# Performance work log

Measured on AMD Instinct MI355X. Metric: run time of the kernel, lower is better.

## Reference

```python
import jax, jax.numpy as jnp
import numpy as np

BLOCK_SIZE = 32
# E2M1 (FP4) representable magnitudes and rounding midpoints
FP4_GRID = jnp.array([0.0, 0.5, 1.0, 1.5, 2.0, 3.0, 4.0, 6.0], dtype=jnp.float32)
FP4_MIDS = jnp.array([0.25, 0.75, 1.25, 1.75, 2.5, 3.5, 5.0], dtype=jnp.float32)


def quantize_to_mxfp4(w, block_size=BLOCK_SIZE):
    """Quantize (K, N) weight to MXFP4: per-block-of-32 (along K) power-of-2 scale
    + E2M1 codes. Returns dequantized-code tensor q (K//bs, bs, N) and scales
    (K//bs, 1, N) so that dequant = q * scales."""
    K, N = w.shape
    wb = w.reshape(K // block_size, block_size, N)
    amax = jnp.max(jnp.abs(wb), axis=1, keepdims=True)          # (K//bs, 1, N)
    # E8M0 scale: 2^(floor(log2(amax)) - 2) so amax/scale falls in [4, 8) -> clipped to 6
    exp = jnp.floor(jnp.log2(jnp.maximum(amax, 1e-30))) - 2.0
    scales = jnp.exp2(exp)
    x = wb / scales
    idx = jnp.digitize(jnp.abs(x), FP4_MIDS)                    # round-to-nearest FP4 magnitude
    q = jnp.sign(x) * FP4_GRID[idx]
    return q, scales


def mxfp4_matmul(inputs, q, scales, block_size=BLOCK_SIZE):
    """inputs: (..., K); q: (K//bs, bs, N); scales: (K//bs, 1, N)."""
    K = inputs.shape[-1]
    N = q.shape[-1]
    w = (q * scales).reshape(K, N)   # fused dequant (reference form)
    return inputs @ w


def setup_inputs() -> dict:
    key = jax.random.key(0)
    ks = jax.random.split(key, 3)
    B, S, D, F = 4, 2048, 2048, 8192
    inputs = jax.random.normal(ks[0], (B, S, D), dtype=jnp.float32)
    up_kernel = jax.random.normal(ks[1], (D, F), dtype=jnp.float32) * (1.0 / np.sqrt(D))
    down_kernel = jax.random.normal(ks[2], (F, D), dtype=jnp.float32) * (1.0 / np.sqrt(F))
    up_bias = jnp.zeros((F,), dtype=jnp.float32)
    down_bias = jnp.zeros((D,), dtype=jnp.float32)
    return {"inputs": inputs, "up_kernel": up_kernel, "up_bias": up_bias,
            "down_kernel": down_kernel, "down_bias": down_bias}


def reference(inputs, up_kernel, up_bias, down_kernel, down_bias):
    q_up, s_up = quantize_to_mxfp4(up_kernel, BLOCK_SIZE)
    x = mxfp4_matmul(inputs, q_up, s_up, BLOCK_SIZE) + up_bias
    x = jax.nn.gelu(x)
    q_dn, s_dn = quantize_to_mxfp4(down_kernel, BLOCK_SIZE)
    x = mxfp4_matmul(x, q_dn, s_dn, BLOCK_SIZE) + down_bias
    return x
```

## Files before the change

kernel.cpp:

```cpp
#include <hip/hip_runtime.h>
#include <hip/hip_bf16.h>

typedef __bf16 bf16_t;
typedef __attribute__((ext_vector_type(8))) __bf16 bf16x8;
typedef __attribute__((ext_vector_type(4))) float f32x4;
typedef __attribute__((ext_vector_type(4))) unsigned int u32x4;

__device__ __forceinline__ void gload_lds16(const bf16_t* g, bf16_t* l) {
    __builtin_amdgcn_global_load_lds(
        (const __attribute__((address_space(1))) void*)g,
        (__attribute__((address_space(3))) void*)l,
        16, 0, 0);
}

__device__ __forceinline__ float gelu_f(float v) {
    float u = 0.7978845608028654f * (v + 0.044715f * v * v * v);
    float e = __expf(-2.f * u);
    float t = __fdividef(1.f - e, 1.f + e);
    return 0.5f * v * (1.f + t);
}

__global__ void cvt_kernel(const float* __restrict__ in, bf16_t* __restrict__ out, int n) {
    int i = (blockIdx.x * blockDim.x + threadIdx.x) << 3;
    if (i >= n) return;
    const f32x4* p = (const f32x4*)(in + i);
    f32x4 a = __builtin_nontemporal_load(p);
    f32x4 b = __builtin_nontemporal_load(p + 1);
    bf16x8 o;
    o[0] = (bf16_t)a[0]; o[1] = (bf16_t)a[1]; o[2] = (bf16_t)a[2]; o[3] = (bf16_t)a[3];
    o[4] = (bf16_t)b[0]; o[5] = (bf16_t)b[1]; o[6] = (bf16_t)b[2]; o[7] = (bf16_t)b[3];
    *(bf16x8*)(out + i) = o;
}

__global__ void quantize_kernel(const float* __restrict__ w, bf16_t* __restrict__ wt,
                                int K, int N) {
    int tid = blockIdx.x * blockDim.x + threadIdx.x;
    int total = (K >> 5) * N;
    if (tid >= total) return;
    int n = tid % N;
    int b = tid / N;
    const float* src = w + (size_t)b * 32 * N + n;
    float v[32];
    float amax = 0.f;
#pragma unroll
    for (int i = 0; i < 32; ++i) {
        v[i] = __builtin_nontemporal_load(src + (size_t)i * N);
        amax = fmaxf(amax, fabsf(v[i]));
    }
    unsigned eb = (__float_as_uint(amax) >> 23) & 0xFF;
    float scale = __uint_as_float((eb - 2u) << 23);
    float inv   = __uint_as_float((256u - eb) << 23);
    if (amax == 0.f) { scale = 0.f; inv = 0.f; }
    bf16_t dq[32];
#pragma unroll
    for (int i = 0; i < 32; ++i) {
        float x  = v[i] * inv;
        float ax = fabsf(x);
        float q = ax < 0.25f ? 0.0f : ax < 0.75f ? 0.5f : ax < 1.25f ? 1.0f :
                  ax < 1.75f ? 1.5f : ax < 2.5f  ? 2.0f : ax < 3.5f  ? 3.0f :
                  ax < 5.0f  ? 4.0f : 6.0f;
        float d = copysignf(q * scale, x);
        dq[i] = (bf16_t)d;
    }
    bf16_t* dst = wt + (size_t)n * K + b * 32;
#pragma unroll
    for (int j = 0; j < 4; ++j) {
        bf16x8 p;
#pragma unroll
        for (int t = 0; t < 8; ++t) p[t] = dq[j * 8 + t];
        *(bf16x8*)(dst + j * 8) = p;
    }
}

#define VMW4  asm volatile("s_waitcnt vmcnt(4)" ::: "memory")
#define VMW0  asm volatile("s_waitcnt vmcnt(0)" ::: "memory")
#define BARR  asm volatile("s_barrier" ::: "memory")
#define LGKM0 asm volatile("s_waitcnt lgkmcnt(0)" ::: "memory")

#define MFMA_ROW(MI, A0, A1)                                                          \
    acc[MI][0] = __builtin_amdgcn_mfma_f32_16x16x32_bf16(A0, bf00, acc[MI][0],0,0,0); \
    acc[MI][0] = __builtin_amdgcn_mfma_f32_16x16x32_bf16(A1, bf01, acc[MI][0],0,0,0); \
    acc[MI][1] = __builtin_amdgcn_mfma_f32_16x16x32_bf16(A0, bf10, acc[MI][1],0,0,0); \
    acc[MI][1] = __builtin_amdgcn_mfma_f32_16x16x32_bf16(A1, bf11, acc[MI][1],0,0,0); \
    acc[MI][2] = __builtin_amdgcn_mfma_f32_16x16x32_bf16(A0, bf20, acc[MI][2],0,0,0); \
    acc[MI][2] = __builtin_amdgcn_mfma_f32_16x16x32_bf16(A1, bf21, acc[MI][2],0,0,0); \
    acc[MI][3] = __builtin_amdgcn_mfma_f32_16x16x32_bf16(A0, bf30, acc[MI][3],0,0,0); \
    acc[MI][3] = __builtin_amdgcn_mfma_f32_16x16x32_bf16(A1, bf31, acc[MI][3],0,0,0);

#define PHASE(BUF, P, STAGE_STMT, TAIL_STMT)                                          \
  {                                                                                   \
    af00 = lda(BUF, 2*(P),   0); af01 = lda(BUF, 2*(P),   1);                         \
    af10 = lda(BUF, 2*(P)+1, 0); af11 = lda(BUF, 2*(P)+1, 1);                         \
    if ((P) == 0) {                                                                   \
      bf00 = ldb(BUF,0,0); bf01 = ldb(BUF,0,1);                                       \
      bf10 = ldb(BUF,1,0); bf11 = ldb(BUF,1,1);                                       \
      bf20 = ldb(BUF,2,0); bf21 = ldb(BUF,2,1);                                       \
      bf30 = ldb(BUF,3,0); bf31 = ldb(BUF,3,1);                                       \
    }                                                                                 \
    STAGE_STMT;                                                                       \
    BARR;                                                                             \
    LGKM0;                                                                            \
    __builtin_amdgcn_s_setprio(1);                                                    \
    MFMA_ROW(2*(P),   af00, af01);                                                    \
    MFMA_ROW(2*(P)+1, af10, af11);                                                    \
    __builtin_amdgcn_s_setprio(0);                                                    \
    TAIL_STMT;                                                                        \
    BARR;                                                                             \
  }

template <int EPI, int MAP>
__global__ __launch_bounds__(512, 2)
void gemm_kernel(const bf16_t* __restrict__ A, const bf16_t* __restrict__ Bt,
                 const float* __restrict__ bias, void* __restrict__ Cout,
                 int M, int N, int K) {
    __shared__ __align__(16) char smem[131072];
    bf16_t* sAp = (bf16_t*)smem;
    bf16_t* sBp = (bf16_t*)(smem + 65536);
    const int tid     = threadIdx.x;
    const int lane    = tid & 63;
    const int wv      = tid >> 6;
    const int wr      = wv >> 2;
    const int wc      = wv & 3;
    const int laneLow = lane & 15;
    const int laneHi  = lane >> 4;

    int bm, bn;
    const int bid = blockIdx.x;
    if (MAP == 1) {
        const int xcd = bid & 7;
        const int l   = bid >> 3;
        const int r   = l >> 5;
        const int u   = l & 31;
        bm = r * 8 + ((xcd >> 2) << 2) + (u >> 3);
        bn = ((xcd & 3) << 3) + (u & 7);
    } else {
        const int ntn = N >> 8;
        const int nwg = gridDim.x;
        int wg  = (bid & 7) * (nwg >> 3) + (bid >> 3);
        bm = wg / ntn; bn = wg % ntn;
    }

    const int sr8 = lane >> 3;
    const int swz = (((lane & 7) ^ sr8) << 3);
    const bf16_t* aSrc = A  + (size_t)(bm * 256 + wv * 8 + sr8) * K + swz;
    const bf16_t* bSrc = Bt + (size_t)(bn * 256 + wv * 8 + sr8) * K + swz;

    auto stageA = [&](int b, int kt, int h) {
        const bf16_t* s = aSrc + (size_t)(h * 128) * K + kt * 64;
        gload_lds16(s,                &sAp[b * 16384 + (h * 128 + wv * 8) * 64]);
        gload_lds16(s + (size_t)64*K, &sAp[b * 16384 + (h * 128 + 64 + wv * 8) * 64]);
    };
    auto stageB = [&](int b, int kt, int h) {
        const bf16_t* s = bSrc + (size_t)(h * 128) * K + kt * 64;
        gload_lds16(s,                &sBp[b * 16384 + (h * 128 + wv * 8) * 64]);
        gload_lds16(s + (size_t)64*K, &sBp[b * 16384 + (h * 128 + 64 + wv * 8) * 64]);
    };

    const int s7  = laneLow & 7;
    const int xk0 = ((laneHi) ^ s7) << 3;
    const int xk1 = ((4 + laneHi) ^ s7) << 3;
    const int aOffBase = (wr * 128 + laneLow) * 64;
    const int bOffBase = (wc * 64 + laneLow) * 64;
    auto lda = [&](int b, int m, int ks) -> bf16x8 {
        return *(const bf16x8*)(&sAp[b * 16384 + aOffBase + m * 1024 + (ks ? xk1 : xk0)]);
    };
    auto ldb = [&](int b, int n2, int ks) -> bf16x8 {
        return *(const bf16x8*)(&sBp[b * 16384 + bOffBase + n2 * 1024 + (ks ? xk1 : xk0)]);
    };

    f32x4 acc[8][4];
#pragma unroll
    for (int i = 0; i < 8; ++i)
#pragma unroll
        for (int j = 0; j < 4; ++j) acc[i][j] = (f32x4){0.f, 0.f, 0.f, 0.f};

    bf16x8 af00, af01, af10, af11;
    bf16x8 bf00, bf01, bf10, bf11, bf20, bf21, bf30, bf31;

    stageA(0, 0, 0); stageA(0, 0, 1);
    stageB(0, 0, 0); stageB(0, 0, 1);
    stageB(1, 1, 0); stageB(1, 1, 1);
    VMW4;
    BARR;

    const int niter = K >> 7;
    for (int i = 0; i < niter; ++i) {
        const bool nlast = (i + 1 < niter);
        const int kO  = 2 * i + 1;
        const int kN  = 2 * i + 2;
        const int kN1 = 2 * i + 3;
        PHASE(0, 0, stageA(1, kO, 0), ((void)0));
        PHASE(0, 1, stageA(1, kO, 1), ((void)0));
        PHASE(0, 2, if (nlast) stageB(0, kN, 0), ((void)0));
        PHASE(0, 3, if (nlast) stageB(0, kN, 1),
              if (nlast) { VMW4; } else { VMW0; });
        PHASE(1, 0, if (nlast) stageA(0, kN, 0), ((void)0));
        PHASE(1, 1, if (nlast) stageA(0, kN, 1), ((void)0));
        PHASE(1, 2, if (nlast) stageB(1, kN1, 0), ((void)0));
        PHASE(1, 3, if (nlast) stageB(1, kN1, 1),
              if (nlast) { VMW4; });
    }

    if (EPI == 0) {
        bf16_t* sC = (bf16_t*)smem;
#pragma unroll
        for (int n = 0; n < 4; ++n) {
            const int colL = wc * 64 + n * 16 + laneLow;
            const float bv = bias[bn * 256 + colL];
#pragma unroll
            for (int m = 0; m < 8; ++m) {
#pragma unroll
                for (int j = 0; j < 4; ++j) {
                    const int rowL = wr * 128 + m * 16 + (laneHi << 2) + j;
                    float v = acc[m][n][j] + bv;
                    int byte = (rowL << 9) + (colL << 1);
                    byte ^= ((rowL >> 2) & 3) << 5;
                    *(bf16_t*)((char*)sC + byte) = (bf16_t)gelu_f(v);
                }
            }
        }
        LGKM0;
        BARR;
        bf16_t* Cb = (bf16_t*)Cout;
        const size_t rb = (size_t)bm * 256, cb = (size_t)bn * 256;
#pragma unroll
        for (int s = 0; s < 16; ++s) {
            const int row = s * 16 + (tid >> 5);
            int byte = (row << 9) + ((tid & 31) << 4);
            byte ^= ((row >> 2) & 3) << 5;
            u32x4 v = *(const u32x4*)((char*)sC + byte);
            __builtin_nontemporal_store(
                v, (u32x4*)(&Cb[(rb + row) * N + cb + ((tid & 31) << 3)]));
        }
    } else {
        const int r0 = bm * 256 + wr * 128 + (laneHi << 2);
        const int c0 = bn * 256 + wc * 64 + laneLow;
        float* Cf = (float*)Cout;
#pragma unroll
        for (int n = 0; n < 4; ++n) {
            const int col = c0 + n * 16;
            const float bv = bias[col];
#pragma unroll
            for (int m = 0; m < 8; ++m) {
#pragma unroll
                for (int j = 0; j < 4; ++j) {
                    const int row = r0 + m * 16 + j;
                    __builtin_nontemporal_store(acc[m][n][j] + bv,
                                                &Cf[(size_t)row * N + col]);
                }
            }
        }
    }
}

extern "C" void kernel_launch(void* const* d_in, const int* in_sizes, int n_in,
                              void* d_out, int out_size, void* d_ws, size_t ws_size,
                              hipStream_t stream) {
    const float* inputs = (const float*)d_in[0];
    const float* up_w   = (const float*)d_in[1];
    const float* up_b   = (const float*)d_in[2];
    const float* dn_w   = (const float*)d_in[3];
    const float* dn_b   = (const float*)d_in[4];
    float* out = (float*)d_out;

    const int D = in_sizes[4];
    const int F = in_sizes[2];
    const int M = in_sizes[0] / D;

    size_t r0_bytes = (size_t)(M > F ? M : F) * D * 2;
    char* ws = (char*)d_ws;
    bf16_t* in_bf = (bf16_t*)ws;
    bf16_t* wdn_t = (bf16_t*)ws;
    bf16_t* wup_t = (bf16_t*)(ws + r0_bytes);
    bf16_t* mid   = (bf16_t*)(ws + r0_bytes + (size_t)F * D * 2);

    int ncvt = M * D;
    cvt_kernel<<<(ncvt / 8 + 255) / 256, 256, 0, stream>>>(inputs, in_bf, ncvt);
    int qup = (D / 32) * F;
    quantize_kernel<<<(qup + 255) / 256, 256, 0, stream>>>(up_w, wup_t, D, F);
    gemm_kernel<0, 1><<<(M / 256) * (F / 256), 512, 0, stream>>>(
        in_bf, wup_t, up_b, (void*)mid, M, F, D);
    int qdn = (F / 32) * D;
    quantize_kernel<<<(qdn + 255) / 256, 256, 0, stream>>>(dn_w, wdn_t, F, D);
    gemm_kernel<1, 0><<<(M / 256) * (D / 256), 512, 0, stream>>>(
        mid, wdn_t, dn_b, (void*)out, M, D, F);
}
```

Measured before the change: 548.1 us.

## Fuse prep kernels and overlap down-weight quantization with up GEMM

Merges the input bf16 conversion and up-weight quantization into one launch. The down-weight quantization now runs as 512 extra workgroups appended to the up-projection GEMM grid, writing to a separate workspace region so it can overlap with the GEMM instead of running as its own serial kernel. This removes two launches and the idle gap between them. In exchange, the extra blocks compete with the GEMM for CUs, use a lot of workspace, and could delay GEMM tail blocks or change their scheduling order.

After: 555.6 us. No clear change (+1.4%).

```diff
diff --git a/kernel.cpp b/kernel.cpp
--- a/kernel.cpp
+++ b/kernel.cpp
@@ -20,25 +20,11 @@
     return 0.5f * v * (1.f + t);
 }
 
-__global__ void cvt_kernel(const float* __restrict__ in, bf16_t* __restrict__ out, int n) {
-    int i = (blockIdx.x * blockDim.x + threadIdx.x) << 3;
-    if (i >= n) return;
-    const f32x4* p = (const f32x4*)(in + i);
-    f32x4 a = __builtin_nontemporal_load(p);
-    f32x4 b = __builtin_nontemporal_load(p + 1);
-    bf16x8 o;
-    o[0] = (bf16_t)a[0]; o[1] = (bf16_t)a[1]; o[2] = (bf16_t)a[2]; o[3] = (bf16_t)a[3];
-    o[4] = (bf16_t)b[0]; o[5] = (bf16_t)b[1]; o[6] = (bf16_t)b[2]; o[7] = (bf16_t)b[3];
-    *(bf16x8*)(out + i) = o;
-}
-
-__global__ void quantize_kernel(const float* __restrict__ w, bf16_t* __restrict__ wt,
-                                int K, int N) {
-    int tid = blockIdx.x * blockDim.x + threadIdx.x;
-    int total = (K >> 5) * N;
-    if (tid >= total) return;
-    int n = tid % N;
-    int b = tid / N;
+__device__ __forceinline__ void quant_one(const float* __restrict__ w,
+                                          bf16_t* __restrict__ wt,
+                                          int K, int N, int tix) {
+    int n = tix % N;
+    int b = tix / N;
     const float* src = w + (size_t)b * 32 * N + n;
     float v[32];
     float amax = 0.f;
@@ -69,6 +55,28 @@
 #pragma unroll
         for (int t = 0; t < 8; ++t) p[t] = dq[j * 8 + t];
         *(bf16x8*)(dst + j * 8) = p;
+    }
+}
+
+__global__ void prep_kernel(const float* __restrict__ in, bf16_t* __restrict__ out,
+                            int ncvt, int cvtBlocks,
+                            const float* __restrict__ upw, bf16_t* __restrict__ upwt,
+                            int K, int N) {
+    int bid = blockIdx.x;
+    if (bid < cvtBlocks) {
+        int i = (bid * blockDim.x + threadIdx.x) << 3;
+        if (i >= ncvt) return;
+        const f32x4* p = (const f32x4*)(in + i);
+        f32x4 a = __builtin_nontemporal_load(p);
+        f32x4 b = __builtin_nontemporal_load(p + 1);
+        bf16x8 o;
+        o[0] = (bf16_t)a[0]; o[1] = (bf16_t)a[1]; o[2] = (bf16_t)a[2]; o[3] = (bf16_t)a[3];
+        o[4] = (bf16_t)b[0]; o[5] = (bf16_t)b[1]; o[6] = (bf16_t)b[2]; o[7] = (bf16_t)b[3];
+        *(bf16x8*)(out + i) = o;
+    } else {
+        int tix = (bid - cvtBlocks) * blockDim.x + threadIdx.x;
+        if (tix >= (K >> 5) * N) return;
+        quant_one(upw, upwt, K, N, tix);
     }
 }
 
@@ -108,15 +116,26 @@
     BARR;                                                                             \
   }
 
-template <int EPI, int MAP>
+template <int EPI, int MAP, int XQ>
 __global__ __launch_bounds__(512, 2)
 void gemm_kernel(const bf16_t* __restrict__ A, const bf16_t* __restrict__ Bt,
                  const float* __restrict__ bias, void* __restrict__ Cout,
-                 int M, int N, int K) {
+                 int M, int N, int K,
+                 const float* __restrict__ qw, bf16_t* __restrict__ qwt,
+                 int qK, int qN, int gemmBlocks) {
     __shared__ __align__(16) char smem[131072];
+    const int tid = threadIdx.x;
+
+    if (XQ && (int)blockIdx.x >= gemmBlocks) {
+        const int total  = (qK >> 5) * qN;
+        const int stride = (gridDim.x - gemmBlocks) * 512;
+        for (int tix = (blockIdx.x - gemmBlocks) * 512 + tid; tix < total; tix += stride)
+            quant_one(qw, qwt, qK, qN, tix);
+        return;
+    }
+
     bf16_t* sAp = (bf16_t*)smem;
     bf16_t* sBp = (bf16_t*)(smem + 65536);
-    const int tid     = threadIdx.x;
     const int lane    = tid & 63;
     const int wv      = tid >> 6;
     const int wr      = wv >> 2;
@@ -135,7 +154,7 @@
         bn = ((xcd & 3) << 3) + (u & 7);
     } else {
         const int ntn = N >> 8;
-        const int nwg = gridDim.x;
+        const int nwg = gemmBlocks;
         int wg  = (bid & 7) * (nwg >> 3) + (bid >> 3);
         bm = wg / ntn; bn = wg % ntn;
     }
@@ -275,13 +294,19 @@
     bf16_t* mid   = (bf16_t*)(ws + r0_bytes + (size_t)F * D * 2);
 
     int ncvt = M * D;
-    cvt_kernel<<<(ncvt / 8 + 255) / 256, 256, 0, stream>>>(inputs, in_bf, ncvt);
-    int qup = (D / 32) * F;
-    quantize_kernel<<<(qup + 255) / 256, 256, 0, stream>>>(up_w, wup_t, D, F);
-    gemm_kernel<0, 1><<<(M / 256) * (F / 256), 512, 0, stream>>>(
-        in_bf, wup_t, up_b, (void*)mid, M, F, D);
-    int qdn = (F / 32) * D;
-    quantize_kernel<<<(qdn + 255) / 256, 256, 0, stream>>>(dn_w, wdn_t, F, D);
-    gemm_kernel<1, 0><<<(M / 256) * (D / 256), 512, 0, stream>>>(
-        mid, wdn_t, dn_b, (void*)out, M, D, F);
-}
+    int cvtBlocks = ncvt / (8 * 256);
+    int qupBlocks = ((D / 32) * F + 255) / 256;
+    prep_kernel<<<cvtBlocks + qupBlocks, 256, 0, stream>>>(
+        inputs, in_bf, ncvt, cvtBlocks, up_w, wup_t, D, F);
+
+    int gemmBlocks = (M / 256) * (F / 256);
+    bf16_t* wdn_t2 = (bf16_t*)(ws + r0_bytes + (size_t)F * D * 2 + (size_t)M * F * 2);
+    gemm_kernel<0, 1, 1><<<gemmBlocks + 512, 512, 0, stream>>>(
+        in_bf, wup_t, up_b, (void*)mid, M, F, D,
+        dn_w, wdn_t2, F, D, gemmBlocks);
+
+    gemm_kernel<1, 0, 0><<<(M / 256) * (D / 256), 512, 0, stream>>>(
+        mid, wdn_t2, dn_b, (void*)out, M, D, F,
+        nullptr, nullptr, 0, 0, 256);
+    (void)wdn_t; (void)ws_size; (void)n_in; (void)out_size;
+}
```

## Merge prep kernels and make up-projection GEMM persistent over M segments

Applied to the files above, without the earlier changes.

The cast and both weight quantizations are merged into one prep launch, with the down weights moved to their own workspace region so they no longer alias the input buffer. The first GEMM becomes a persistent kernel of 256 blocks. Each block keeps a fixed N column tile and its B stream across four M tiles, with an XCD-aware mapping, and writes GELU output after every 16 K-iterations. The aim is fewer launches and better B reuse in L2. In exchange, the epilogue now does direct scattered 2-byte nontemporal stores instead of the LDS-staged 16-byte stores, which risks poorer write coalescing. The persistent kernel also hardcodes the loop counts and grid size to the test shapes.

Measured after the change: 556.4 us. About the same (+1.5%).

```diff
diff --git a/kernel.cpp b/kernel.cpp
--- a/kernel.cpp
+++ b/kernel.cpp
@@ -20,25 +20,11 @@
     return 0.5f * v * (1.f + t);
 }
 
-__global__ void cvt_kernel(const float* __restrict__ in, bf16_t* __restrict__ out, int n) {
-    int i = (blockIdx.x * blockDim.x + threadIdx.x) << 3;
-    if (i >= n) return;
-    const f32x4* p = (const f32x4*)(in + i);
-    f32x4 a = __builtin_nontemporal_load(p);
-    f32x4 b = __builtin_nontemporal_load(p + 1);
-    bf16x8 o;
-    o[0] = (bf16_t)a[0]; o[1] = (bf16_t)a[1]; o[2] = (bf16_t)a[2]; o[3] = (bf16_t)a[3];
-    o[4] = (bf16_t)b[0]; o[5] = (bf16_t)b[1]; o[6] = (bf16_t)b[2]; o[7] = (bf16_t)b[3];
-    *(bf16x8*)(out + i) = o;
-}
-
-__global__ void quantize_kernel(const float* __restrict__ w, bf16_t* __restrict__ wt,
-                                int K, int N) {
-    int tid = blockIdx.x * blockDim.x + threadIdx.x;
-    int total = (K >> 5) * N;
-    if (tid >= total) return;
-    int n = tid % N;
-    int b = tid / N;
+__device__ __forceinline__ void quant_one(const float* __restrict__ w,
+                                          bf16_t* __restrict__ wt,
+                                          int K, int N, int tix) {
+    int n = tix % N;
+    int b = tix / N;
     const float* src = w + (size_t)b * 32 * N + n;
     float v[32];
     float amax = 0.f;
@@ -69,6 +55,34 @@
 #pragma unroll
         for (int t = 0; t < 8; ++t) p[t] = dq[j * 8 + t];
         *(bf16x8*)(dst + j * 8) = p;
+    }
+}
+
+__global__ void prep_kernel(const float* __restrict__ in, bf16_t* __restrict__ out,
+                            int ncvt, int cvtB,
+                            const float* __restrict__ upw, bf16_t* __restrict__ upwt,
+                            int upK, int upN, int qupB,
+                            const float* __restrict__ dnw, bf16_t* __restrict__ dnwt,
+                            int dnK, int dnN) {
+    int bid = blockIdx.x;
+    if (bid < cvtB) {
+        int i = (bid * blockDim.x + threadIdx.x) << 3;
+        if (i >= ncvt) return;
+        const f32x4* p = (const f32x4*)(in + i);
+        f32x4 a = __builtin_nontemporal_load(p);
+        f32x4 b = __builtin_nontemporal_load(p + 1);
+        bf16x8 o;
+        o[0] = (bf16_t)a[0]; o[1] = (bf16_t)a[1]; o[2] = (bf16_t)a[2]; o[3] = (bf16_t)a[3];
+        o[4] = (bf16_t)b[0]; o[5] = (bf16_t)b[1]; o[6] = (bf16_t)b[2]; o[7] = (bf16_t)b[3];
+        *(bf16x8*)(out + i) = o;
+    } else if (bid < cvtB + qupB) {
+        int tix = (bid - cvtB) * blockDim.x + threadIdx.x;
+        if (tix >= (upK >> 5) * upN) return;
+        quant_one(upw, upwt, upK, upN, tix);
+    } else {
+        int tix = (bid - cvtB - qupB) * blockDim.x + threadIdx.x;
+        if (tix >= (dnK >> 5) * dnN) return;
+        quant_one(dnw, dnwt, dnK, dnN, tix);
     }
 }
 
@@ -108,6 +122,110 @@
     BARR;                                                                             \
   }
 
+__global__ __launch_bounds__(512, 2)
+void gemm1_persistent(const bf16_t* __restrict__ A, const bf16_t* __restrict__ Bt,
+                      const float* __restrict__ bias, bf16_t* __restrict__ C,
+                      int M, int N, int K) {
+    __shared__ __align__(16) char smem[131072];
+    bf16_t* sAp = (bf16_t*)smem;
+    bf16_t* sBp = (bf16_t*)(smem + 65536);
+    const int tid     = threadIdx.x;
+    const int lane    = tid & 63;
+    const int wv      = tid >> 6;
+    const int wr      = wv >> 2;
+    const int wc      = wv & 3;
+    const int laneLow = lane & 15;
+    const int laneHi  = lane >> 4;
+
+    const int bid = blockIdx.x;
+    const int xcd = bid & 7, q = bid >> 3;
+    const int bn  = ((xcd & 3) << 3) + (q & 7);
+    const int bm0 = ((xcd >> 2) << 2) + (q >> 3);
+
+    const int sr8 = lane >> 3;
+    const int swz = (((lane & 7) ^ sr8) << 3);
+    const size_t aTh = (size_t)(wv * 8 + sr8) * K + swz;
+    const bf16_t* bSrc = Bt + (size_t)(bn * 256 + wv * 8 + sr8) * K + swz;
+
+    auto stageA = [&](int b, int t, int h) {
+        const bf16_t* s = A + (size_t)(bm0 + ((t >> 5) << 3)) * (size_t)(256 * K)
+                            + aTh + (size_t)(h * 128) * K + (t & 31) * 64;
+        gload_lds16(s,                &sAp[b * 16384 + (h * 128 + wv * 8) * 64]);
+        gload_lds16(s + (size_t)64*K, &sAp[b * 16384 + (h * 128 + 64 + wv * 8) * 64]);
+    };
+    auto stageB = [&](int b, int t, int h) {
+        const bf16_t* s = bSrc + (size_t)(h * 128) * K + (t & 31) * 64;
+        gload_lds16(s,                &sBp[b * 16384 + (h * 128 + wv * 8) * 64]);
+        gload_lds16(s + (size_t)64*K, &sBp[b * 16384 + (h * 128 + 64 + wv * 8) * 64]);
+    };
+
+    const int s7  = laneLow & 7;
+    const int xk0 = ((laneHi) ^ s7) << 3;
+    const int xk1 = ((4 + laneHi) ^ s7) << 3;
+    const int aOffBase = (wr * 128 + laneLow) * 64;
+    const int bOffBase = (wc * 64 + laneLow) * 64;
+    auto lda = [&](int b, int m, int ks) -> bf16x8 {
+        return *(const bf16x8*)(&sAp[b * 16384 + aOffBase + m * 1024 + (ks ? xk1 : xk0)]);
+    };
+    auto ldb = [&](int b, int n2, int ks) -> bf16x8 {
+        return *(const bf16x8*)(&sBp[b * 16384 + bOffBase + n2 * 1024 + (ks ? xk1 : xk0)]);
+    };
+
+    f32x4 acc[8][4];
+#pragma unroll
+    for (int i = 0; i < 8; ++i)
+#pragma unroll
+        for (int j = 0; j < 4; ++j) acc[i][j] = (f32x4){0.f, 0.f, 0.f, 0.f};
+
+    bf16x8 af00, af01, af10, af11;
+    bf16x8 bf00, bf01, bf10, bf11, bf20, bf21, bf30, bf31;
+
+    stageA(0, 0, 0); stageA(0, 0, 1);
+    stageB(0, 0, 0); stageB(0, 0, 1);
+    stageB(1, 1, 0); stageB(1, 1, 1);
+    VMW4;
+    BARR;
+
+    const int c0 = bn * 256 + wc * 64 + laneLow;
+#pragma unroll 1
+    for (int g = 0; g < 64; ++g) {
+        const bool nl = (g < 63);
+        const int tA1 = 2 * g + 1, tN = 2 * g + 2, tN1 = 2 * g + 3;
+        PHASE(0, 0, stageA(1, tA1, 0), ((void)0));
+        PHASE(0, 1, stageA(1, tA1, 1), ((void)0));
+        PHASE(0, 2, if (nl) stageB(0, tN, 0), ((void)0));
+        PHASE(0, 3, if (nl) stageB(0, tN, 1),
+              if (nl) { VMW4; } else { VMW0; });
+        PHASE(1, 0, if (nl) stageA(0, tN, 0), ((void)0));
+        PHASE(1, 1, if (nl) stageA(0, tN, 1), ((void)0));
+        PHASE(1, 2, if (nl) stageB(1, tN1, 0), ((void)0));
+        PHASE(1, 3, if (nl) stageB(1, tN1, 1),
+              if (nl) { VMW4; });
+
+        if ((g & 15) == 15) {
+            const int seg = g >> 4;
+            const int r0 = (bm0 + (seg << 3)) * 256 + wr * 128 + (laneHi << 2);
+#pragma unroll
+            for (int n = 0; n < 4; ++n) {
+                const int col = c0 + n * 16;
+                const float bv = bias[col];
+#pragma unroll
+                for (int m = 0; m < 8; ++m) {
+#pragma unroll
+                    for (int j = 0; j < 4; ++j) {
+                        const int row = r0 + m * 16 + j;
+                        bf16_t h = (bf16_t)gelu_f(acc[m][n][j] + bv);
+                        __builtin_nontemporal_store(
+                            __builtin_bit_cast(short, h),
+                            (short*)&C[(size_t)row * N + col]);
+                    }
+                    acc[m][n] = (f32x4){0.f, 0.f, 0.f, 0.f};
+                }
+            }
+        }
+    }
+}
+
 template <int EPI, int MAP>
 __global__ __launch_bounds__(512, 2)
 void gemm_kernel(const bf16_t* __restrict__ A, const bf16_t* __restrict__ Bt,
@@ -201,38 +319,7 @@
               if (nlast) { VMW4; });
     }
 
-    if (EPI == 0) {
-        bf16_t* sC = (bf16_t*)smem;
-#pragma unroll
-        for (int n = 0; n < 4; ++n) {
-            const int colL = wc * 64 + n * 16 + laneLow;
-            const float bv = bias[bn * 256 + colL];
-#pragma unroll
-            for (int m = 0; m < 8; ++m) {
-#pragma unroll
-                for (int j = 0; j < 4; ++j) {
-                    const int rowL = wr * 128 + m * 16 + (laneHi << 2) + j;
-                    float v = acc[m][n][j] + bv;
-                    int byte = (rowL << 9) + (colL << 1);
-                    byte ^= ((rowL >> 2) & 3) << 5;
-                    *(bf16_t*)((char*)sC + byte) = (bf16_t)gelu_f(v);
-                }
-            }
-        }
-        LGKM0;
-        BARR;
-        bf16_t* Cb = (bf16_t*)Cout;
-        const size_t rb = (size_t)bm * 256, cb = (size_t)bn * 256;
-#pragma unroll
-        for (int s = 0; s < 16; ++s) {
-            const int row = s * 16 + (tid >> 5);
-            int byte = (row << 9) + ((tid & 31) << 4);
-            byte ^= ((row >> 2) & 3) << 5;
-            u32x4 v = *(const u32x4*)((char*)sC + byte);
-            __builtin_nontemporal_store(
-                v, (u32x4*)(&Cb[(rb + row) * N + cb + ((tid & 31) << 3)]));
-        }
-    } else {
+    {
         const int r0 = bm * 256 + wr * 128 + (laneHi << 2);
         const int c0 = bn * 256 + wc * 64 + laneLow;
         float* Cf = (float*)Cout;
@@ -270,18 +357,23 @@
     size_t r0_bytes = (size_t)(M > F ? M : F) * D * 2;
     char* ws = (char*)d_ws;
     bf16_t* in_bf = (bf16_t*)ws;
-    bf16_t* wdn_t = (bf16_t*)ws;
     bf16_t* wup_t = (bf16_t*)(ws + r0_bytes);
     bf16_t* mid   = (bf16_t*)(ws + r0_bytes + (size_t)F * D * 2);
+    bf16_t* wdn_t = (bf16_t*)(ws + r0_bytes + (size_t)F * D * 2 + (size_t)M * F * 2);
 
     int ncvt = M * D;
-    cvt_kernel<<<(ncvt / 8 + 255) / 256, 256, 0, stream>>>(inputs, in_bf, ncvt);
-    int qup = (D / 32) * F;
-    quantize_kernel<<<(qup + 255) / 256, 256, 0, stream>>>(up_w, wup_t, D, F);
-    gemm_kernel<0, 1><<<(M / 256) * (F / 256), 512, 0, stream>>>(
-        in_bf, wup_t, up_b, (void*)mid, M, F, D);
-    int qdn = (F / 32) * D;
-    quantize_kernel<<<(qdn + 255) / 256, 256, 0, stream>>>(dn_w, wdn_t, F, D);
+    int cvtB = ncvt / (8 * 256);
+    int qupB = ((D / 32) * F + 255) / 256;
+    int qdnB = ((F / 32) * D + 255) / 256;
+    prep_kernel<<<cvtB + qupB + qdnB, 256, 0, stream>>>(
+        inputs, in_bf, ncvt, cvtB,
+        up_w, wup_t, D, F, qupB,
+        dn_w, wdn_t, F, D);
+
+    gemm1_persistent<<<256, 512, 0, stream>>>(
+        in_bf, wup_t, up_b, mid, M, F, D);
+
     gemm_kernel<1, 0><<<(M / 256) * (D / 256), 512, 0, stream>>>(
         mid, wdn_t, dn_b, (void*)out, M, D, F);
-}
+    (void)ws_size; (void)n_in; (void)out_size;
+}
```

## Switch GEMM to 32x32x16 MFMA tiles and merge prep kernels into one launch

Applied to the files above, without the earlier changes.

The GEMM inner loop moves from 16x16x32 bf16 MFMAs to 32x32x16 MFMAs. Each wave's 128x64 tile is now 4x2 blocks of 32x32, which cuts LDS fragment reads per MFMA FLOP and changes the LDS read addressing and the epilogue row mapping. The input cast and both weight quantizations now run in a single prep kernel, saving launches and letting the down-weight quantize overlap the other prep work. The cost is a separate workspace region for the down weights, plus a risk of LDS bank conflicts under the new swizzle use.

Measured after the change: 589.6 us. 7.6% more time.

```diff
diff --git a/kernel.cpp b/kernel.cpp
--- a/kernel.cpp
+++ b/kernel.cpp
@@ -4,6 +4,7 @@
 typedef __bf16 bf16_t;
 typedef __attribute__((ext_vector_type(8))) __bf16 bf16x8;
 typedef __attribute__((ext_vector_type(4))) float f32x4;
+typedef __attribute__((ext_vector_type(16))) float f32x16;
 typedef __attribute__((ext_vector_type(4))) unsigned int u32x4;
 
 __device__ __forceinline__ void gload_lds16(const bf16_t* g, bf16_t* l) {
@@ -20,25 +21,11 @@
     return 0.5f * v * (1.f + t);
 }
 
-__global__ void cvt_kernel(const float* __restrict__ in, bf16_t* __restrict__ out, int n) {
-    int i = (blockIdx.x * blockDim.x + threadIdx.x) << 3;
-    if (i >= n) return;
-    const f32x4* p = (const f32x4*)(in + i);
-    f32x4 a = __builtin_nontemporal_load(p);
-    f32x4 b = __builtin_nontemporal_load(p + 1);
-    bf16x8 o;
-    o[0] = (bf16_t)a[0]; o[1] = (bf16_t)a[1]; o[2] = (bf16_t)a[2]; o[3] = (bf16_t)a[3];
-    o[4] = (bf16_t)b[0]; o[5] = (bf16_t)b[1]; o[6] = (bf16_t)b[2]; o[7] = (bf16_t)b[3];
-    *(bf16x8*)(out + i) = o;
-}
-
-__global__ void quantize_kernel(const float* __restrict__ w, bf16_t* __restrict__ wt,
-                                int K, int N) {
-    int tid = blockIdx.x * blockDim.x + threadIdx.x;
-    int total = (K >> 5) * N;
-    if (tid >= total) return;
-    int n = tid % N;
-    int b = tid / N;
+__device__ __forceinline__ void quant_one(const float* __restrict__ w,
+                                          bf16_t* __restrict__ wt,
+                                          int K, int N, int tix) {
+    int n = tix % N;
+    int b = tix / N;
     const float* src = w + (size_t)b * 32 * N + n;
     float v[32];
     float amax = 0.f;
@@ -72,37 +59,61 @@
     }
 }
 
+__global__ void prep_kernel(const float* __restrict__ in, bf16_t* __restrict__ out,
+                            int ncvt, int cvtB,
+                            const float* __restrict__ upw, bf16_t* __restrict__ upwt,
+                            int upK, int upN, int qupB,
+                            const float* __restrict__ dnw, bf16_t* __restrict__ dnwt,
+                            int dnK, int dnN) {
+    int bid = blockIdx.x;
+    if (bid < cvtB) {
+        int i = (bid * blockDim.x + threadIdx.x) << 3;
+        if (i >= ncvt) return;
+        const f32x4* p = (const f32x4*)(in + i);
+        f32x4 a = __builtin_nontemporal_load(p);
+        f32x4 b = __builtin_nontemporal_load(p + 1);
+        bf16x8 o;
+        o[0] = (bf16_t)a[0]; o[1] = (bf16_t)a[1]; o[2] = (bf16_t)a[2]; o[3] = (bf16_t)a[3];
+        o[4] = (bf16_t)b[0]; o[5] = (bf16_t)b[1]; o[6] = (bf16_t)b[2]; o[7] = (bf16_t)b[3];
+        *(bf16x8*)(out + i) = o;
+    } else if (bid < cvtB + qupB) {
+        int tix = (bid - cvtB) * blockDim.x + threadIdx.x;
+        if (tix >= (upK >> 5) * upN) return;
+        quant_one(upw, upwt, upK, upN, tix);
+    } else {
+        int tix = (bid - cvtB - qupB) * blockDim.x + threadIdx.x;
+        if (tix >= (dnK >> 5) * dnN) return;
+        quant_one(dnw, dnwt, dnK, dnN, tix);
+    }
+}
+
 #define VMW4  asm volatile("s_waitcnt vmcnt(4)" ::: "memory")
 #define VMW0  asm volatile("s_waitcnt vmcnt(0)" ::: "memory")
 #define BARR  asm volatile("s_barrier" ::: "memory")
 #define LGKM0 asm volatile("s_waitcnt lgkmcnt(0)" ::: "memory")
 
-#define MFMA_ROW(MI, A0, A1)                                                          \
-    acc[MI][0] = __builtin_amdgcn_mfma_f32_16x16x32_bf16(A0, bf00, acc[MI][0],0,0,0); \
-    acc[MI][0] = __builtin_amdgcn_mfma_f32_16x16x32_bf16(A1, bf01, acc[MI][0],0,0,0); \
-    acc[MI][1] = __builtin_amdgcn_mfma_f32_16x16x32_bf16(A0, bf10, acc[MI][1],0,0,0); \
-    acc[MI][1] = __builtin_amdgcn_mfma_f32_16x16x32_bf16(A1, bf11, acc[MI][1],0,0,0); \
-    acc[MI][2] = __builtin_amdgcn_mfma_f32_16x16x32_bf16(A0, bf20, acc[MI][2],0,0,0); \
-    acc[MI][2] = __builtin_amdgcn_mfma_f32_16x16x32_bf16(A1, bf21, acc[MI][2],0,0,0); \
-    acc[MI][3] = __builtin_amdgcn_mfma_f32_16x16x32_bf16(A0, bf30, acc[MI][3],0,0,0); \
-    acc[MI][3] = __builtin_amdgcn_mfma_f32_16x16x32_bf16(A1, bf31, acc[MI][3],0,0,0);
+#define MFMA32(A, B, C) __builtin_amdgcn_mfma_f32_32x32x16_bf16(A, B, C, 0, 0, 0)
 
 #define PHASE(BUF, P, STAGE_STMT, TAIL_STMT)                                          \
   {                                                                                   \
-    af00 = lda(BUF, 2*(P),   0); af01 = lda(BUF, 2*(P),   1);                         \
-    af10 = lda(BUF, 2*(P)+1, 0); af11 = lda(BUF, 2*(P)+1, 1);                         \
+    af0 = lda(BUF, P, 0); af1 = lda(BUF, P, 1);                                       \
+    af2 = lda(BUF, P, 2); af3 = lda(BUF, P, 3);                                       \
     if ((P) == 0) {                                                                   \
-      bf00 = ldb(BUF,0,0); bf01 = ldb(BUF,0,1);                                       \
-      bf10 = ldb(BUF,1,0); bf11 = ldb(BUF,1,1);                                       \
-      bf20 = ldb(BUF,2,0); bf21 = ldb(BUF,2,1);                                       \
-      bf30 = ldb(BUF,3,0); bf31 = ldb(BUF,3,1);                                       \
+      bf00 = ldb(BUF,0,0); bf01 = ldb(BUF,0,1); bf02 = ldb(BUF,0,2); bf03 = ldb(BUF,0,3); \
+      bf10 = ldb(BUF,1,0); bf11 = ldb(BUF,1,1); bf12 = ldb(BUF,1,2); bf13 = ldb(BUF,1,3); \
     }                                                                                 \
     STAGE_STMT;                                                                       \
     BARR;                                                                             \
     LGKM0;                                                                            \
     __builtin_amdgcn_s_setprio(1);                                                    \
-    MFMA_ROW(2*(P),   af00, af01);                                                    \
-    MFMA_ROW(2*(P)+1, af10, af11);                                                    \
+    acc[P][0] = MFMA32(af0, bf00, acc[P][0]);                                         \
+    acc[P][1] = MFMA32(af0, bf10, acc[P][1]);                                         \
+    acc[P][0] = MFMA32(af1, bf01, acc[P][0]);                                         \
+    acc[P][1] = MFMA32(af1, bf11, acc[P][1]);                                         \
+    acc[P][0] = MFMA32(af2, bf02, acc[P][0]);                                         \
+    acc[P][1] = MFMA32(af2, bf12, acc[P][1]);                                         \
+    acc[P][0] = MFMA32(af3, bf03, acc[P][0]);                                         \
+    acc[P][1] = MFMA32(af3, bf13, acc[P][1]);                                         \
     __builtin_amdgcn_s_setprio(0);                                                    \
     TAIL_STMT;                                                                        \
     BARR;                                                                             \
@@ -116,13 +127,13 @@
     __shared__ __align__(16) char smem[131072];
     bf16_t* sAp = (bf16_t*)smem;
     bf16_t* sBp = (bf16_t*)(smem + 65536);
-    const int tid     = threadIdx.x;
-    const int lane    = tid & 63;
-    const int wv      = tid >> 6;
-    const int wr      = wv >> 2;
-    const int wc      = wv & 3;
-    const int laneLow = lane & 15;
-    const int laneHi  = lane >> 4;
+    const int tid    = threadIdx.x;
+    const int lane   = tid & 63;
+    const int wv     = tid >> 6;
+    const int wr     = wv >> 2;
+    const int wc     = wv & 3;
+    const int lane31 = lane & 31;
+    const int laneHi2 = lane >> 5;
 
     int bm, bn;
     const int bid = blockIdx.x;
@@ -156,26 +167,28 @@
         gload_lds16(s + (size_t)64*K, &sBp[b * 16384 + (h * 128 + 64 + wv * 8) * 64]);
     };
 
-    const int s7  = laneLow & 7;
-    const int xk0 = ((laneHi) ^ s7) << 3;
-    const int xk1 = ((4 + laneHi) ^ s7) << 3;
-    const int aOffBase = (wr * 128 + laneLow) * 64;
-    const int bOffBase = (wc * 64 + laneLow) * 64;
-    auto lda = [&](int b, int m, int ks) -> bf16x8 {
-        return *(const bf16x8*)(&sAp[b * 16384 + aOffBase + m * 1024 + (ks ? xk1 : xk0)]);
+    const int s7 = lane31 & 7;
+    auto lda = [&](int b, int mt, int k) -> bf16x8 {
+        const int row = wr * 128 + mt * 32 + lane31;
+        const int up  = ((2 * k + laneHi2) ^ s7) << 3;
+        return *(const bf16x8*)(&sAp[b * 16384 + row * 64 + up]);
     };
-    auto ldb = [&](int b, int n2, int ks) -> bf16x8 {
-        return *(const bf16x8*)(&sBp[b * 16384 + bOffBase + n2 * 1024 + (ks ? xk1 : xk0)]);
+    auto ldb = [&](int b, int nt, int k) -> bf16x8 {
+        const int row = wc * 64 + nt * 32 + lane31;
+        const int up  = ((2 * k + laneHi2) ^ s7) << 3;
+        return *(const bf16x8*)(&sBp[b * 16384 + row * 64 + up]);
     };
 
-    f32x4 acc[8][4];
-#pragma unroll
-    for (int i = 0; i < 8; ++i)
-#pragma unroll
-        for (int j = 0; j < 4; ++j) acc[i][j] = (f32x4){0.f, 0.f, 0.f, 0.f};
-
-    bf16x8 af00, af01, af10, af11;
-    bf16x8 bf00, bf01, bf10, bf11, bf20, bf21, bf30, bf31;
+    f32x16 acc[4][2];
+#pragma unroll
+    for (int i = 0; i < 4; ++i)
+#pragma unroll
+        for (int j = 0; j < 2; ++j)
+#pragma unroll
+            for (int e = 0; e < 16; ++e) acc[i][j][e] = 0.f;
+
+    bf16x8 af0, af1, af2, af3;
+    bf16x8 bf00, bf01, bf02, bf03, bf10, bf11, bf12, bf13;
 
     stageA(0, 0, 0); stageA(0, 0, 1);
     stageB(0, 0, 0); stageB(0, 0, 1);
@@ -204,15 +217,16 @@
     if (EPI == 0) {
         bf16_t* sC = (bf16_t*)smem;
 #pragma unroll
-        for (int n = 0; n < 4; ++n) {
-            const int colL = wc * 64 + n * 16 + laneLow;
+        for (int nt = 0; nt < 2; ++nt) {
+            const int colL = wc * 64 + nt * 32 + lane31;
             const float bv = bias[bn * 256 + colL];
 #pragma unroll
-            for (int m = 0; m < 8; ++m) {
-#pragma unroll
-                for (int j = 0; j < 4; ++j) {
-                    const int rowL = wr * 128 + m * 16 + (laneHi << 2) + j;
-                    float v = acc[m][n][j] + bv;
+            for (int mt = 0; mt < 4; ++mt) {
+#pragma unroll
+                for (int r = 0; r < 16; ++r) {
+                    const int rowL = wr * 128 + mt * 32 + (r & 3) + 8 * (r >> 2)
+                                     + 4 * laneHi2;
+                    float v = acc[mt][nt][r] + bv;
                     int byte = (rowL << 9) + (colL << 1);
                     byte ^= ((rowL >> 2) & 3) << 5;
                     *(bf16_t*)((char*)sC + byte) = (bf16_t)gelu_f(v);
@@ -233,19 +247,18 @@
                 v, (u32x4*)(&Cb[(rb + row) * N + cb + ((tid & 31) << 3)]));
         }
     } else {
-        const int r0 = bm * 256 + wr * 128 + (laneHi << 2);
-        const int c0 = bn * 256 + wc * 64 + laneLow;
         float* Cf = (float*)Cout;
 #pragma unroll
-        for (int n = 0; n < 4; ++n) {
-            const int col = c0 + n * 16;
+        for (int nt = 0; nt < 2; ++nt) {
+            const int col = bn * 256 + wc * 64 + nt * 32 + lane31;
             const float bv = bias[col];
 #pragma unroll
-            for (int m = 0; m < 8; ++m) {
-#pragma unroll
-                for (int j = 0; j < 4; ++j) {
-                    const int row = r0 + m * 16 + j;
-                    __builtin_nontemporal_store(acc[m][n][j] + bv,
+            for (int mt = 0; mt < 4; ++mt) {
+#pragma unroll
+                for (int r = 0; r < 16; ++r) {
+                    const int row = bm * 256 + wr * 128 + mt * 32 + (r & 3)
+                                    + 8 * (r >> 2) + 4 * laneHi2;
+                    __builtin_nontemporal_store(acc[mt][nt][r] + bv,
                                                 &Cf[(size_t)row * N + col]);
                 }
             }
@@ -270,18 +283,23 @@
     size_t r0_bytes = (size_t)(M > F ? M : F) * D * 2;
     char* ws = (char*)d_ws;
     bf16_t* in_bf = (bf16_t*)ws;
-    bf16_t* wdn_t = (bf16_t*)ws;
     bf16_t* wup_t = (bf16_t*)(ws + r0_bytes);
     bf16_t* mid   = (bf16_t*)(ws + r0_bytes + (size_t)F * D * 2);
+    bf16_t* wdn_t = (bf16_t*)(ws + r0_bytes + (size_t)F * D * 2 + (size_t)M * F * 2);
 
     int ncvt = M * D;
-    cvt_kernel<<<(ncvt / 8 + 255) / 256, 256, 0, stream>>>(inputs, in_bf, ncvt);
-    int qup = (D / 32) * F;
-    quantize_kernel<<<(qup + 255) / 256, 256, 0, stream>>>(up_w, wup_t, D, F);
+    int cvtB = ncvt / (8 * 256);
+    int qupB = ((D / 32) * F + 255) / 256;
+    int qdnB = ((F / 32) * D + 255) / 256;
+    prep_kernel<<<cvtB + qupB + qdnB, 256, 0, stream>>>(
+        inputs, in_bf, ncvt, cvtB,
+        up_w, wup_t, D, F, qupB,
+        dn_w, wdn_t, F, D);
+
     gemm_kernel<0, 1><<<(M / 256) * (F / 256), 512, 0, stream>>>(
         in_bf, wup_t, up_b, (void*)mid, M, F, D);
-    int qdn = (F / 32) * D;
-    quantize_kernel<<<(qdn + 255) / 256, 256, 0, stream>>>(dn_w, wdn_t, F, D);
+
     gemm_kernel<1, 0><<<(M / 256) * (D / 256), 512, 0, stream>>>(
         mid, wdn_t, dn_b, (void*)out, M, D, F);
-}
+    (void)ws_size; (void)n_in; (void)out_size;
+}
```
